# Kernel tuning notes

Hardware: AMD Instinct MI355X
Metric: run time of the kernel (lower is better)

The kernel has to match this reference:

```python
import jax, jax.numpy as jnp
import numpy as np

N, L, IN, H1, H2, OUT = 256, 2048, 8, 256, 128, 1


def setup_inputs() -> dict:
    key = jax.random.key(0)
    ks = jax.random.split(key, 9)
    s1 = 1.0 / np.sqrt(H1)  # torch LSTMCell/Linear init scale
    s2 = 1.0 / np.sqrt(H2)
    u = lambda k, shape, s: jax.random.uniform(k, shape, jnp.float32, -s, s)
    return {
        "x": jax.random.normal(ks[0], (N, L, IN), jnp.float32),
        "W_ih": u(ks[1], (4 * H1, IN + 1), s1),
        "W_hh": u(ks[2], (4 * H1, H1), s1),
        "b_ih": u(ks[3], (4 * H1,), s1),
        "b_hh": u(ks[4], (4 * H1,), s1),
        "W1": u(ks[5], (H2, H1), s1),
        "b1": u(ks[6], (H2,), s1),
        "W2": u(ks[7], (OUT, H2), s2),
        "b2": u(ks[8], (OUT,), s2),
    }


def reference(x, W_ih, W_hh, b_ih, b_hh, W1, b1, W2, b2):
    # Dropout is identity at inference (eval mode); initial_output = 0.
    n = x.shape[0]
    h0 = jnp.zeros((n, H1), x.dtype)
    c0 = jnp.zeros((n, H1), x.dtype)
    p0 = jnp.zeros((n, OUT), x.dtype)  # prev_output

    def step(carry, x_t):
        hx, cx, prev = carry
        inp_t = jnp.concatenate([x_t, prev], axis=-1)          # [N, IN+1]
        gates = inp_t @ W_ih.T + b_ih + hx @ W_hh.T + b_hh     # [N, 4*H1]
        i, f, g, o = jnp.split(gates, 4, axis=-1)              # torch gate order i,f,g,o
        i = jax.nn.sigmoid(i)
        f = jax.nn.sigmoid(f)
        g = jnp.tanh(g)
        o = jax.nn.sigmoid(o)
        cx = f * cx + i * g
        hx = o * jnp.tanh(cx)
        out = jax.nn.relu(hx @ W1.T + b1) @ W2.T + b2          # [N, OUT]
        return (hx, cx, out), (out, cx)

    _, (outs, cells) = jax.lax.scan(step, (h0, c0, p0), jnp.swapaxes(x, 0, 1))
    output = jnp.swapaxes(outs, 0, 1)       # [N, L, OUT]
    cell_states = jnp.swapaxes(cells, 0, 1)  # [N, L, H1]
    return (output, cell_states)
```

## Files before the change

kernel.cpp:

```cpp
#include <hip/hip_runtime.h>


typedef __attribute__((ext_vector_type(8))) short short8;
typedef __attribute__((ext_vector_type(4))) float f32x4;
typedef __attribute__((ext_vector_type(2))) float f32x2;

#define LSEQ 2048

__device__ __forceinline__ unsigned short f2bf(float f) {
  unsigned int u = __float_as_uint(f);
  return (unsigned short)((u + 0x7FFFu + ((u >> 16) & 1u)) >> 16);
}
__device__ __forceinline__ float sigm(float x) {
  float e = __builtin_amdgcn_exp2f(-1.44269504089f * x);
  return __builtin_amdgcn_rcpf(1.0f + e);
}
__device__ __forceinline__ float tanh_(float x) {
  float ax = __builtin_fabsf(x);
  float e = __builtin_amdgcn_exp2f(-2.88539008178f * ax);
  float t = (1.0f - e) * __builtin_amdgcn_rcpf(1.0f + e);
  return __builtin_copysignf(t, x);
}
__device__ __forceinline__ void wg_barrier() {
  __asm__ __volatile__("s_waitcnt lgkmcnt(0)" ::: "memory");
  __builtin_amdgcn_s_barrier();
}

__global__ void prep_kernel(const float* __restrict__ W_ih, const float* __restrict__ W_hh,
                            const float* __restrict__ b_ih, const float* __restrict__ b_hh,
                            const float* __restrict__ W1,
                            unsigned short* __restrict__ wstream,
                            unsigned short* __restrict__ w1stream,
                            float* __restrict__ bias,
                            unsigned long long* __restrict__ packets) {
  int tid = blockIdx.x * 256 + threadIdx.x;
  if (tid < 36864) {
    int f = tid >> 6, l = tid & 63;
    int w = f / 72, rem = f % 72, nt = rem / 9, kt = rem % 9;
    int g = (nt >> 1) * 256 + w * 32 + (nt & 1) * 16 + (l & 15);
    int k0 = kt * 32 + (l >> 4) * 8;
    unsigned short* dst = wstream + (size_t)f * 512 + l * 8;
#pragma unroll
    for (int j = 0; j < 8; j++) {
      int k = k0 + j;
      float v;
      if (k < 256)       v = W_hh[g * 256 + k];
      else if (k < 264)  v = W_ih[g * 9 + (k - 256)];
      else               v = 0.0f;
      dst[j] = f2bf(v);
    }
  } else if (tid < 36864 + 4096) {
    int t2 = tid - 36864;
    int f = t2 >> 6, l = t2 & 63;
    int w = f >> 3, kt = f & 7;
    int h2 = w * 16 + (l & 15);
    int k0 = kt * 32 + (l >> 4) * 8;
    unsigned short* dst = w1stream + (size_t)f * 512 + l * 8;
#pragma unroll
    for (int j = 0; j < 8; j++) dst[j] = f2bf(W1[h2 * 256 + k0 + j]);
  } else if (tid < 36864 + 4096 + 1024) {
    int g = tid - 36864 - 4096;
    bias[g] = b_ih[g] + b_hh[g];
  } else if (tid < 36864 + 4096 + 1024 + 65536) {
    packets[tid - 41984] = 0ull;
  }
}

__global__ __launch_bounds__(512, 2) void lstm_main(
    const float* __restrict__ x, const float* __restrict__ W_ih,
    const float* __restrict__ b1, const float* __restrict__ W2, const float* __restrict__ b2,
    const unsigned short* __restrict__ wstream, const unsigned short* __restrict__ w1stream,
    const float* __restrict__ bias,
    unsigned long long* __restrict__ packets,
    float* __restrict__ out0, float* __restrict__ out1) {
  __shared__ unsigned short A[2][16][296];
  __shared__ float gbuf[4][16][34];
  __shared__ float part[8][17];

  const int tid = threadIdx.x;
  const int w = tid >> 6, l = tid & 63, lr = l & 15, lg = l >> 4;
  const int bg = blockIdx.x & 15, sl = blockIdx.x >> 4;
  const int n0 = bg * 16, u0 = sl * 32;

  short8 wg_[9], w1_[8];
  {
    const short8* wp = (const short8*)wstream;
    const short8* w1p = (const short8*)w1stream;
#pragma unroll
    for (int kt = 0; kt < 9; kt++) wg_[kt] = wp[(size_t)((sl * 8 + w) * 9 + kt) * 64 + l];
#pragma unroll
    for (int kt = 0; kt < 8; kt++) w1_[kt] = w1p[(size_t)(w * 8 + kt) * 64 + l];
  }
  const float biasv = bias[(w >> 1) * 256 + u0 + (w & 1) * 16 + lr];
  const float b1v = b1[w * 16 + lr];
  const float w2v = W2[w * 16 + lr];
  const float b2v = b2[0];

  const int cs = tid >> 4, cu2 = (tid & 15) * 2;
  float wpv[8];
  float c0r = 0.f, c1r = 0.f;
  if (tid < 256) {
#pragma unroll
    for (int g = 0; g < 4; g++) {
      wpv[g * 2 + 0] = W_ih[(g * 256 + u0 + cu2) * 9 + 8];
      wpv[g * 2 + 1] = W_ih[(g * 256 + u0 + cu2 + 1) * 9 + 8];
    }
  }

  for (int i = tid; i < 2 * 16 * 296; i += 512) ((unsigned short*)A)[i] = 0;

  f32x4 xv = {0.f, 0.f, 0.f, 0.f};
  if (w == sl && l < 32)
    xv = *(const f32x4*)(x + (size_t)(n0 + (l >> 1)) * LSEQ * 8 + (l & 1) * 4);

  __syncthreads();

  for (int k = 0; k <= LSEQ; k++) {
    const int slot = k & 1;

    if (w == sl) {
      if (l < 32 && k < LSEQ) {
        unsigned long long xp = (unsigned long long)f2bf(xv.x)
                              | ((unsigned long long)f2bf(xv.y) << 16)
                              | ((unsigned long long)f2bf(xv.z) << 32)
                              | ((unsigned long long)f2bf(xv.w) << 48);
        *(unsigned long long*)&A[slot][l >> 1][256 + (l & 1) * 4] = xp;
        if (k + 1 < LSEQ)
          xv = *(const f32x4*)(x + ((size_t)(n0 + (l >> 1)) * LSEQ + (k + 1)) * 8 + (l & 1) * 4);
      }
    } else if (k > 0) {
      const unsigned long long* pk = packets + (((size_t)slot * 16 + bg) * 8 + w) * 256 + l * 4;
      unsigned long long v[4];
#pragma unroll
      for (int i = 0; i < 4; i++)
        v[i] = __hip_atomic_load(&pk[i], __ATOMIC_RELAXED, __HIP_MEMORY_SCOPE_AGENT);
#pragma unroll
      for (int i = 0; i < 4; i++)
        while ((unsigned)(v[i] & 0xFFFFu) != (unsigned)k)
          v[i] = __hip_atomic_load(&pk[i], __ATOMIC_RELAXED, __HIP_MEMORY_SCOPE_AGENT);
#pragma unroll
      for (int i = 0; i < 4; i++) {
        int W = l * 4 + i, s = W >> 4, pr = W & 15;
        *(unsigned int*)&A[slot][s][w * 32 + pr * 2] = (unsigned int)(v[i] >> 16);
      }
    }
    wg_barrier();

    short8 afr[9];
#pragma unroll
    for (int kt = 0; kt < 9; kt++)
      afr[kt] = *(const short8*)&A[slot][lr][kt * 32 + lg * 8];
    if (k < LSEQ) {
      f32x4 acc = {biasv, biasv, biasv, biasv};
#pragma unroll
      for (int kt = 0; kt < 9; kt++)
        acc = __builtin_amdgcn_mfma_f32_16x16x32_bf16(afr[kt], wg_[kt], acc, 0, 0, 0);
#pragma unroll
      for (int r = 0; r < 4; r++) gbuf[w >> 1][lg * 4 + r][(w & 1) * 16 + lr] = acc[r];
    }
    if (k > 0) {
      f32x4 m = {b1v, b1v, b1v, b1v};
#pragma unroll
      for (int kt = 0; kt < 8; kt++)
        m = __builtin_amdgcn_mfma_f32_16x16x32_bf16(afr[kt], w1_[kt], m, 0, 0, 0);
      float p[4];
#pragma unroll
      for (int r = 0; r < 4; r++) {
        float v = m[r] > 0.f ? m[r] : 0.f;
        p[r] = v * w2v;
        p[r] += __shfl_xor(p[r], 1, 64);
        p[r] += __shfl_xor(p[r], 2, 64);
        p[r] += __shfl_xor(p[r], 4, 64);
        p[r] += __shfl_xor(p[r], 8, 64);
      }
      if (lr == 0) {
#pragma unroll
        for (int r = 0; r < 4; r++) part[w][lg * 4 + r] = p[r];
      }
    }
    wg_barrier();

    if (tid < 256) {
      float o = 0.f;
      if (k > 0) {
        o = b2v;
#pragma unroll
        for (int i = 0; i < 8; i++) o += part[i][cs];
        if (cu2 == 0 && sl == 0)
          __builtin_nontemporal_store(o, out0 + (size_t)(n0 + cs) * LSEQ + (k - 1));
      }
      if (k < LSEQ) {
        float gi0 = gbuf[0][cs][cu2] + wpv[0] * o, gi1 = gbuf[0][cs][cu2 + 1] + wpv[1] * o;
        float gf0 = gbuf[1][cs][cu2] + wpv[2] * o, gf1 = gbuf[1][cs][cu2 + 1] + wpv[3] * o;
        float gg0 = gbuf[2][cs][cu2] + wpv[4] * o, gg1 = gbuf[2][cs][cu2 + 1] + wpv[5] * o;
        float go0 = gbuf[3][cs][cu2] + wpv[6] * o, go1 = gbuf[3][cs][cu2 + 1] + wpv[7] * o;
        c0r = sigm(gf0) * c0r + sigm(gi0) * tanh_(gg0);
        c1r = sigm(gf1) * c1r + sigm(gi1) * tanh_(gg1);
        float h0 = sigm(go0) * tanh_(c0r);
        float h1 = sigm(go1) * tanh_(c1r);
        f32x2 cv = {c0r, c1r};
        __builtin_nontemporal_store(cv,
            (f32x2*)(out1 + ((size_t)(n0 + cs) * LSEQ + k) * 256 + u0 + cu2));
        unsigned int hb0 = f2bf(h0), hb1 = f2bf(h1);
        unsigned long long wv = (unsigned long long)(unsigned)(k + 1)
                              | ((unsigned long long)hb0 << 16)
                              | ((unsigned long long)hb1 << 32);
        unsigned long long* dst =
            packets + (((size_t)((k + 1) & 1) * 16 + bg) * 8 + sl) * 256 + tid;
        __hip_atomic_store(dst, wv, __ATOMIC_RELAXED, __HIP_MEMORY_SCOPE_AGENT);
        *(unsigned int*)&A[slot ^ 1][cs][u0 + cu2] = hb0 | (hb1 << 16);
      }
    }
  }
}

extern "C" void kernel_launch(void* const* d_in, const int* in_sizes, int n_in,
                              void* d_out, int out_size, void* d_ws, size_t ws_size,
                              hipStream_t stream) {
  const float* x    = (const float*)d_in[0];
  const float* W_ih = (const float*)d_in[1];
  const float* W_hh = (const float*)d_in[2];
  const float* b_ih = (const float*)d_in[3];
  const float* b_hh = (const float*)d_in[4];
  const float* W1   = (const float*)d_in[5];
  const float* b1   = (const float*)d_in[6];
  const float* W2   = (const float*)d_in[7];
  const float* b2   = (const float*)d_in[8];

  unsigned short*     wstream  = (unsigned short*)d_ws;
  unsigned short*     w1stream = (unsigned short*)((char*)d_ws + 1179648);
  float*              bias     = (float*)((char*)d_ws + 1179648 + 65536);
  unsigned long long* packets  = (unsigned long long*)((char*)d_ws + 1249280);

  float* out0 = (float*)d_out;
  float* out1 = out0 + 256 * LSEQ;

  prep_kernel<<<420, 256, 0, stream>>>(W_ih, W_hh, b_ih, b_hh, W1, wstream, w1stream, bias, packets);
  lstm_main<<<128, 512, 0, stream>>>(x, W_ih, b1, W2, b2, wstream, w1stream, bias, packets,
                                     out0, out1);
}
```

Before: 5.940 ms.

## Add fast sc0-path packet exchange with fallback and remap blocks to batch groups

Each h-packet is now written twice: to a fast buffer using sc0 stores (likely staying in a nearer cache level when the communicating blocks share an XCD) and to the existing agent-scope buffer. Readers poll the fast buffer with a bounded retry budget and fall back permanently to the agent-scope path if polling stalls. The block-to-batch-group mapping is changed so that blocks exchanging data are more likely to land together. Packet polling is moved onto warps 4-7, leaving warps 0-3 free. The aim is lower cross-block synchronization latency per timestep, at the cost of a doubled store volume and a coherence assumption that may not hold.

New measurement: 8.308 ms. 39.9% more time.

```diff
diff --git a/kernel.cpp b/kernel.cpp
--- a/kernel.cpp
+++ b/kernel.cpp
@@ -32,7 +32,7 @@
                             unsigned short* __restrict__ wstream,
                             unsigned short* __restrict__ w1stream,
                             float* __restrict__ bias,
-                            unsigned long long* __restrict__ packets) {
+                            unsigned long long* __restrict__ pkts) {
   int tid = blockIdx.x * 256 + threadIdx.x;
   if (tid < 36864) {
     int f = tid >> 6, l = tid & 63;
@@ -61,8 +61,8 @@
   } else if (tid < 36864 + 4096 + 1024) {
     int g = tid - 36864 - 4096;
     bias[g] = b_ih[g] + b_hh[g];
-  } else if (tid < 36864 + 4096 + 1024 + 65536) {
-    packets[tid - 41984] = 0ull;
+  } else if (tid < 36864 + 4096 + 1024 + 131072) {
+    pkts[tid - 41984] = 0ull;
   }
 }
 
@@ -71,7 +71,7 @@
     const float* __restrict__ b1, const float* __restrict__ W2, const float* __restrict__ b2,
     const unsigned short* __restrict__ wstream, const unsigned short* __restrict__ w1stream,
     const float* __restrict__ bias,
-    unsigned long long* __restrict__ packets,
+    unsigned long long* __restrict__ pktF, unsigned long long* __restrict__ pktS,
     float* __restrict__ out0, float* __restrict__ out1) {
   __shared__ unsigned short A[2][16][296];
   __shared__ float gbuf[4][16][34];
@@ -79,7 +79,8 @@
 
   const int tid = threadIdx.x;
   const int w = tid >> 6, l = tid & 63, lr = l & 15, lg = l >> 4;
-  const int bg = blockIdx.x & 15, sl = blockIdx.x >> 4;
+  const int sl = blockIdx.x >> 4;
+  const int bg = (blockIdx.x & 7) * 2 + ((blockIdx.x >> 3) & 1);
   const int n0 = bg * 16, u0 = sl * 32;
 
   short8 wg_[9], w1_[8];
@@ -110,16 +111,18 @@
   for (int i = tid; i < 2 * 16 * 296; i += 512) ((unsigned short*)A)[i] = 0;
 
   f32x4 xv = {0.f, 0.f, 0.f, 0.f};
-  if (w == sl && l < 32)
+  if (w == 7 && l < 32)
     xv = *(const f32x4*)(x + (size_t)(n0 + (l >> 1)) * LSEQ * 8 + (l & 1) * 4);
+
+  bool fastOK = true;
 
   __syncthreads();
 
   for (int k = 0; k <= LSEQ; k++) {
     const int slot = k & 1;
 
-    if (w == sl) {
-      if (l < 32 && k < LSEQ) {
+    if (w >= 4) {
+      if (w == 7 && l < 32 && k < LSEQ) {
         unsigned long long xp = (unsigned long long)f2bf(xv.x)
                               | ((unsigned long long)f2bf(xv.y) << 16)
                               | ((unsigned long long)f2bf(xv.z) << 32)
@@ -128,20 +131,58 @@
         if (k + 1 < LSEQ)
           xv = *(const f32x4*)(x + ((size_t)(n0 + (l >> 1)) * LSEQ + (k + 1)) * 8 + (l & 1) * 4);
       }
-    } else if (k > 0) {
-      const unsigned long long* pk = packets + (((size_t)slot * 16 + bg) * 8 + w) * 256 + l * 4;
-      unsigned long long v[4];
-#pragma unroll
-      for (int i = 0; i < 4; i++)
-        v[i] = __hip_atomic_load(&pk[i], __ATOMIC_RELAXED, __HIP_MEMORY_SCOPE_AGENT);
-#pragma unroll
-      for (int i = 0; i < 4; i++)
-        while ((unsigned)(v[i] & 0xFFFFu) != (unsigned)k)
-          v[i] = __hip_atomic_load(&pk[i], __ATOMIC_RELAXED, __HIP_MEMORY_SCOPE_AGENT);
-#pragma unroll
-      for (int i = 0; i < 4; i++) {
-        int W = l * 4 + i, s = W >> 4, pr = W & 15;
-        *(unsigned int*)&A[slot][s][w * 32 + pr * 2] = (unsigned int)(v[i] >> 16);
+      if (k > 0) {
+        const int m0 = (w - 4) * 2, mcnt = (w == 7) ? 1 : 2;
+        for (int mi = 0; mi < mcnt; mi++) {
+          const int m = m0 + mi;
+          const int rs = m + (m >= sl ? 1 : 0);
+          const size_t pb = (((size_t)slot * 16 + bg) * 8 + rs) * 256 + l * 4;
+          const unsigned long long* pf = pktF + pb;
+          const unsigned long long* ps = pktS + pb;
+          unsigned long long v[4] = {~0ull, ~0ull, ~0ull, ~0ull};
+          bool have = false;
+          if (fastOK) {
+            __asm__ __volatile__(
+                "global_load_dwordx2 %0, %4, off sc0\n\t"
+                "global_load_dwordx2 %1, %4, off offset:8 sc0\n\t"
+                "global_load_dwordx2 %2, %4, off offset:16 sc0\n\t"
+                "global_load_dwordx2 %3, %4, off offset:24 sc0\n\t"
+                "s_waitcnt vmcnt(0)"
+                : "=v"(v[0]), "=v"(v[1]), "=v"(v[2]), "=v"(v[3])
+                : "v"(pf) : "memory");
+            const int budget = (k == 1) ? 4096 : 64;
+            int tries = 0;
+            bool all;
+            for (;;) {
+              all = true;
+#pragma unroll
+              for (int i = 0; i < 4; i++)
+                all = all && ((unsigned)(v[i] & 0xFFFFu) == (unsigned)k);
+              if (all || ++tries > budget) break;
+#pragma unroll
+              for (int i = 0; i < 4; i++)
+                if ((unsigned)(v[i] & 0xFFFFu) != (unsigned)k)
+                  __asm__ __volatile__(
+                      "global_load_dwordx2 %0, %1, off sc0\n\t"
+                      "s_waitcnt vmcnt(0)"
+                      : "=v"(v[i]) : "v"(&pf[i]) : "memory");
+            }
+            bool good = all && (k == 1 || tries <= 16);
+            fastOK = (__all((int)good) != 0);
+            have = all;
+          }
+          if (!have) {
+#pragma unroll
+            for (int i = 0; i < 4; i++)
+              while ((unsigned)(v[i] & 0xFFFFu) != (unsigned)k)
+                v[i] = __hip_atomic_load(&ps[i], __ATOMIC_RELAXED, __HIP_MEMORY_SCOPE_AGENT);
+          }
+#pragma unroll
+          for (int i = 0; i < 4; i++) {
+            int W = l * 4 + i, s = W >> 4, pr = W & 15;
+            *(unsigned int*)&A[slot][s][rs * 32 + pr * 2] = (unsigned int)(v[i] >> 16);
+          }
+        }
       }
     }
     wg_barrier();
@@ -205,9 +246,10 @@
         unsigned long long wv = (unsigned long long)(unsigned)(k + 1)
                               | ((unsigned long long)hb0 << 16)
                               | ((unsigned long long)hb1 << 32);
-        unsigned long long* dst =
-            packets + (((size_t)((k + 1) & 1) * 16 + bg) * 8 + sl) * 256 + tid;
-        __hip_atomic_store(dst, wv, __ATOMIC_RELAXED, __HIP_MEMORY_SCOPE_AGENT);
+        const size_t didx = (((size_t)((k + 1) & 1) * 16 + bg) * 8 + sl) * 256 + tid;
+        __asm__ __volatile__("global_store_dwordx2 %0, %1, off sc0"
+                             :: "v"(pktF + didx), "v"(wv) : "memory");
+        __hip_atomic_store(pktS + didx, wv, __ATOMIC_RELAXED, __HIP_MEMORY_SCOPE_AGENT);
         *(unsigned int*)&A[slot ^ 1][cs][u0 + cu2] = hb0 | (hb1 << 16);
       }
     }
@@ -230,12 +272,13 @@
   unsigned short*     wstream  = (unsigned short*)d_ws;
   unsigned short*     w1stream = (unsigned short*)((char*)d_ws + 1179648);
   float*              bias     = (float*)((char*)d_ws + 1179648 + 65536);
-  unsigned long long* packets  = (unsigned long long*)((char*)d_ws + 1249280);
+  unsigned long long* pktS     = (unsigned long long*)((char*)d_ws + 1249280);
+  unsigned long long* pktF     = (unsigned long long*)((char*)d_ws + 1773568);
 
   float* out0 = (float*)d_out;
   float* out1 = out0 + 256 * LSEQ;
 
-  prep_kernel<<<420, 256, 0, stream>>>(W_ih, W_hh, b_ih, b_hh, W1, wstream, w1stream, bias, packets);
-  lstm_main<<<128, 512, 0, stream>>>(x, W_ih, b1, W2, b2, wstream, w1stream, bias, packets,
+  prep_kernel<<<676, 256, 0, stream>>>(W_ih, W_hh, b_ih, b_hh, W1, wstream, w1stream, bias, pktS);
+  lstm_main<<<128, 512, 0, stream>>>(x, W_ih, b1, W2, b2, wstream, w1stream, bias, pktF, pktS,
                                      out0, out1);
 }
```

## Replace per-word tagged packets with dense hidden-state payload plus per-wave flags

Applied to the files above, without the earlier changes.

Cross-block hidden-state exchange switches from 64-bit packets that each carry a step tag (polled individually) to dense 32-bit bf16 payload stores plus one step-counter flag per wave, written after a vmcnt wait. Consumers spin on four flags with two 64-bit loads, then read the payload with two loads per lane, which halves exchange traffic and cuts the number of polled words. The out0 store is also moved after the critical packet and flag publication. This adds a store-drain wait on the producer and relies on relaxed ordering between the payload and the flag being sufficient.

After: 7.205 ms. 21.3% more time.

```diff
diff --git a/kernel.cpp b/kernel.cpp
--- a/kernel.cpp
+++ b/kernel.cpp
@@ -24,6 +24,12 @@
 __device__ __forceinline__ void wg_barrier() {
   __asm__ __volatile__("s_waitcnt lgkmcnt(0)" ::: "memory");
   __builtin_amdgcn_s_barrier();
+}
+__device__ __forceinline__ unsigned long long agent_load64(const unsigned long long* a) {
+  return __hip_atomic_load(a, __ATOMIC_RELAXED, __HIP_MEMORY_SCOPE_AGENT);
+}
+__device__ __forceinline__ void agent_store32(unsigned int* a, unsigned int v) {
+  __hip_atomic_store(a, v, __ATOMIC_RELAXED, __HIP_MEMORY_SCOPE_AGENT);
 }
 
 __global__ void prep_kernel(const float* __restrict__ W_ih, const float* __restrict__ W_hh,
@@ -32,7 +38,7 @@
                             unsigned short* __restrict__ wstream,
                             unsigned short* __restrict__ w1stream,
                             float* __restrict__ bias,
-                            unsigned long long* __restrict__ packets) {
+                            unsigned int* __restrict__ flags32) {
   int tid = blockIdx.x * 256 + threadIdx.x;
   if (tid < 36864) {
     int f = tid >> 6, l = tid & 63;
@@ -61,8 +67,8 @@
   } else if (tid < 36864 + 4096 + 1024) {
     int g = tid - 36864 - 4096;
     bias[g] = b_ih[g] + b_hh[g];
-  } else if (tid < 36864 + 4096 + 1024 + 65536) {
-    packets[tid - 41984] = 0ull;
+  } else if (tid < 36864 + 4096 + 1024 + 512) {
+    flags32[tid - 41984] = 0u;
   }
 }
 
@@ -71,7 +77,7 @@
     const float* __restrict__ b1, const float* __restrict__ W2, const float* __restrict__ b2,
     const unsigned short* __restrict__ wstream, const unsigned short* __restrict__ w1stream,
     const float* __restrict__ bias,
-    unsigned long long* __restrict__ packets,
+    unsigned long long* __restrict__ packets, unsigned int* __restrict__ flags32,
     float* __restrict__ out0, float* __restrict__ out1) {
   __shared__ unsigned short A[2][16][296];
   __shared__ float gbuf[4][16][34];
@@ -129,20 +135,18 @@
           xv = *(const f32x4*)(x + ((size_t)(n0 + (l >> 1)) * LSEQ + (k + 1)) * 8 + (l & 1) * 4);
       }
     } else if (k > 0) {
-      const unsigned long long* pk = packets + (((size_t)slot * 16 + bg) * 8 + w) * 256 + l * 4;
-      unsigned long long v[4];
-#pragma unroll
-      for (int i = 0; i < 4; i++)
-        v[i] = __hip_atomic_load(&pk[i], __ATOMIC_RELAXED, __HIP_MEMORY_SCOPE_AGENT);
-#pragma unroll
-      for (int i = 0; i < 4; i++)
-        while ((unsigned)(v[i] & 0xFFFFu) != (unsigned)k)
-          v[i] = __hip_atomic_load(&pk[i], __ATOMIC_RELAXED, __HIP_MEMORY_SCOPE_AGENT);
-#pragma unroll
-      for (int i = 0; i < 4; i++) {
-        int W = l * 4 + i, s = W >> 4, pr = W & 15;
-        *(unsigned int*)&A[slot][s][w * 32 + pr * 2] = (unsigned int)(v[i] >> 16);
-      }
+      const unsigned long long* fb = (const unsigned long long*)(flags32 + (bg * 8 + w) * 4);
+      unsigned long long f0, f1;
+      do {
+        f0 = agent_load64(fb);
+        f1 = agent_load64(fb + 1);
+      } while ((unsigned)(f0 & 0xFFFFFFFFu) < (unsigned)k || (unsigned)(f0 >> 32) < (unsigned)k ||
+               (unsigned)(f1 & 0xFFFFFFFFu) < (unsigned)k || (unsigned)(f1 >> 32) < (unsigned)k);
+      const unsigned long long* pk = packets + (((size_t)slot * 16 + bg) * 8 + w) * 128 + l * 2;
+      unsigned long long d0 = agent_load64(pk);
+      unsigned long long d1 = agent_load64(pk + 1);
+      unsigned long long* dst = (unsigned long long*)&A[slot][l >> 2][w * 32 + (l & 3) * 8];
+      dst[0] = d0; dst[1] = d1;
     }
     wg_barrier();
 
@@ -186,8 +190,6 @@
         o = b2v;
 #pragma unroll
         for (int i = 0; i < 8; i++) o += part[i][cs];
-        if (cu2 == 0 && sl == 0)
-          __builtin_nontemporal_store(o, out0 + (size_t)(n0 + cs) * LSEQ + (k - 1));
       }
       if (k < LSEQ) {
         float gi0 = gbuf[0][cs][cu2] + wpv[0] * o, gi1 = gbuf[0][cs][cu2 + 1] + wpv[1] * o;
@@ -198,18 +200,23 @@
         c1r = sigm(gf1) * c1r + sigm(gi1) * tanh_(gg1);
         float h0 = sigm(go0) * tanh_(c0r);
         float h1 = sigm(go1) * tanh_(c1r);
+        unsigned int hb0 = f2bf(h0), hb1 = f2bf(h1);
+        unsigned int hb = hb0 | (hb1 << 16);
+
+        unsigned int* pall = (unsigned int*)(packets +
+            (((size_t)((k + 1) & 1) * 16 + bg) * 8 + sl) * 128);
+        agent_store32(pall + cs * 16 + (cu2 >> 1), hb);
+        __asm__ __volatile__("s_waitcnt vmcnt(0)" ::: "memory");
+        if ((tid & 63) == 0)
+          agent_store32(flags32 + (bg * 8 + sl) * 4 + w, (unsigned)(k + 1));
+
         f32x2 cv = {c0r, c1r};
         __builtin_nontemporal_store(cv,
             (f32x2*)(out1 + ((size_t)(n0 + cs) * LSEQ + k) * 256 + u0 + cu2));
-        unsigned int hb0 = f2bf(h0), hb1 = f2bf(h1);
-        unsigned long long wv = (unsigned long long)(unsigned)(k + 1)
-                              | ((unsigned long long)hb0 << 16)
-                              | ((unsigned long long)hb1 << 32);
-        unsigned long long* dst =
-            packets + (((size_t)((k + 1) & 1) * 16 + bg) * 8 + sl) * 256 + tid;
-        __hip_atomic_store(dst, wv, __ATOMIC_RELAXED, __HIP_MEMORY_SCOPE_AGENT);
-        *(unsigned int*)&A[slot ^ 1][cs][u0 + cu2] = hb0 | (hb1 << 16);
-      }
+        *(unsigned int*)&A[slot ^ 1][cs][u0 + cu2] = hb;
+      }
+      if (k > 0 && cu2 == 0 && sl == 0)
+        __builtin_nontemporal_store(o, out0 + (size_t)(n0 + cs) * LSEQ + (k - 1));
     }
   }
 }
@@ -229,13 +236,15 @@
 
   unsigned short*     wstream  = (unsigned short*)d_ws;
   unsigned short*     w1stream = (unsigned short*)((char*)d_ws + 1179648);
-  float*              bias     = (float*)((char*)d_ws + 1179648 + 65536);
+  float*              bias     = (float*)((char*)d_ws + 1245184);
   unsigned long long* packets  = (unsigned long long*)((char*)d_ws + 1249280);
+  unsigned int*       flags32  = (unsigned int*)((char*)d_ws + 1511424);
 
   float* out0 = (float*)d_out;
   float* out1 = out0 + 256 * LSEQ;
 
-  prep_kernel<<<420, 256, 0, stream>>>(W_ih, W_hh, b_ih, b_hh, W1, wstream, w1stream, bias, packets);
-  lstm_main<<<128, 512, 0, stream>>>(x, W_ih, b1, W2, b2, wstream, w1stream, bias, packets,
-                                     out0, out1);
-}
+  prep_kernel<<<166, 256, 0, stream>>>(W_ih, W_hh, b_ih, b_hh, W1,
+                                       wstream, w1stream, bias, flags32);
+  lstm_main<<<128, 512, 0, stream>>>(x, W_ih, b1, W2, b2, wstream, w1stream, bias,
+                                     packets, flags32, out0, out1);
+}
```
